# Kernel tuning notes

Hardware: AMD Instinct MI355X
Metric: run time of the kernel (lower is better)

The kernel has to match this reference:

```python
import jax, jax.numpy as jnp
import numpy as np

PROJ = 8192     # projDim
THRESH = 1e-8   # numerical-stability epsilon for signed sqrt
L2_EPS = 1e-12  # eps of torch F.normalize


def setup_inputs() -> dict:
    key = jax.random.key(0)
    k1, k2, k3, k4, k5 = jax.random.split(key, 5)
    B, C, H, W = 16, 512, 14, 14
    x = jax.random.normal(k1, (B, C, H, W), dtype=jnp.float32)
    h1 = jax.random.randint(k2, (C,), 0, PROJ, dtype=jnp.int32)
    h2 = jax.random.randint(k3, (C,), 0, PROJ, dtype=jnp.int32)
    s1 = (2 * jax.random.randint(k4, (C,), 0, 2) - 1).astype(jnp.float32)
    s2 = (2 * jax.random.randint(k5, (C,), 0, 2) - 1).astype(jnp.float32)
    return {"x": x, "s1": s1, "s2": s2, "h1": h1, "h2": h2}


def reference(x, s1, s2, h1, h2):
    # x: [B, C, H, W]; h*: [C] hash buckets in [0, PROJ); s*: [C] signs (+-1)
    B, C, H, W = x.shape
    x_flat = jnp.transpose(x, (0, 2, 3, 1)).reshape(-1, C)  # [N, C], N = B*H*W

    def count_sketch(s, h):
        # Equivalent to x_flat @ M with M[c, h[c]] = s[c]: scatter-add of
        # sign-weighted channels into PROJ bins.  -> [N, PROJ]
        return jax.ops.segment_sum((x_flat * s).T, h, num_segments=PROJ).T

    fft1 = jnp.fft.fft(count_sketch(s1, h1), axis=-1)
    fft2 = jnp.fft.fft(count_sketch(s2, h2), axis=-1)
    conv = jnp.fft.ifft(fft1 * fft2, axis=-1).real       # [N, PROJ]
    y = conv.reshape(B, H, W, PROJ).sum(axis=(1, 2))      # sum pool -> [B, PROJ]
    y = jnp.sign(y) * jnp.sqrt(jnp.abs(y) + THRESH)       # signed sqrt
    norm = jnp.linalg.norm(y, axis=1, keepdims=True)
    return y / jnp.maximum(norm, L2_EPS)                  # l2 normalize (dim=1)
```

## Files before the change

kernel.cpp:

```cpp
#include <hip/hip_runtime.h>
#include <math.h>

#define PROJ 8192
#define NB   16
#define NC   512
#define HW   196
#define NKC  7

typedef __attribute__((ext_vector_type(8))) short bf16x8;
typedef __attribute__((ext_vector_type(4))) float f32x4;

__device__ __forceinline__ unsigned bf16_rne(float f) {
    unsigned u = __builtin_bit_cast(unsigned, f);
    return (u + 0x7fffu + ((u >> 16) & 1u)) >> 16;
}

__device__ __forceinline__ void cvt_frag(const float4 f0, const float4 f1,
                                         const float s, bf16x8& hi, bf16x8& lo) {
    const float f[8] = {f0.x * s, f0.y * s, f0.z * s, f0.w * s,
                        f1.x * s, f1.y * s, f1.z * s, f1.w * s};
    bf16x8 h, l;
#pragma unroll
    for (int c = 0; c < 8; ++c) {
        const unsigned hu = bf16_rne(f[c]);
        h[c] = (short)hu;
        l[c] = (short)bf16_rne(f[c] - __builtin_bit_cast(float, hu << 16));
    }
    hi = h;
    lo = l;
}

__global__ __launch_bounds__(512, 2)
void cbp_gram(const float* __restrict__ x,
              const float* __restrict__ s1,
              const float* __restrict__ s2,
              const int*   __restrict__ h1,
              const int*   __restrict__ h2,
              float* __restrict__ ws) {
    __shared__ float sk[PROJ];
    __shared__ int   lh1[128], lh2[128];

    const int tid = threadIdx.x;
    const int blk = blockIdx.x;
    const int b    = 2 * (blk & 7) + (blk >> 7);
    const int tile = (blk >> 3) & 15;
    const int c1base = (tile >> 2) * 128;
    const int c2base = (tile & 3) * 128;

    const int lane = tid & 63;
    const int wave = tid >> 6;
    const int quad = lane >> 4;
    const int l15  = lane & 15;
    const int wr   = (wave >> 1) * 32;
    const int wc   = (wave & 1) * 64;

    for (int i = tid; i < PROJ; i += 512) sk[i] = 0.f;
    if (tid < 128) { lh1[tid] = h1[c1base + tid]; lh2[tid] = h2[c2base + tid]; }

    const float* xa = x + ((size_t)b * NC + c1base) * HW;
    const float* xb = x + ((size_t)b * NC + c2base) * HW;

    const float* pA[2]; float sa[2];
#pragma unroll
    for (int i = 0; i < 2; ++i) {
        const int r = wr + i * 16 + l15;
        pA[i] = xa + r * HW;
        sa[i] = s1[c1base + r];
    }
    const float* pB[4]; float sb[4];
#pragma unroll
    for (int j = 0; j < 4; ++j) {
        const int r = wc + j * 16 + l15;
        pB[j] = xb + r * HW;
        sb[j] = s2[c2base + r];
    }

    f32x4 acc[2][4];
#pragma unroll
    for (int i = 0; i < 2; ++i)
#pragma unroll
        for (int j = 0; j < 4; ++j) acc[i][j] = (f32x4){0.f, 0.f, 0.f, 0.f};

    const float4 z4 = {0.f, 0.f, 0.f, 0.f};
    float4 buf[2][12];

#define LOADC(par, kc) do {                                                   \
    const int kk_ = (kc) * 32 + quad * 8;                                     \
    const bool ok0_ = (kk_ + 3) < HW, ok1_ = (kk_ + 7) < HW;                  \
    _Pragma("unroll") for (int i_ = 0; i_ < 2; ++i_) {                        \
        buf[par][2*i_]   = ok0_ ? *(const float4*)(pA[i_] + kk_)     : z4;    \
        buf[par][2*i_+1] = ok1_ ? *(const float4*)(pA[i_] + kk_ + 4) : z4; }  \
    _Pragma("unroll") for (int j_ = 0; j_ < 4; ++j_) {                        \
        buf[par][4+2*j_]   = ok0_ ? *(const float4*)(pB[j_] + kk_)     : z4;  \
        buf[par][4+2*j_+1] = ok1_ ? *(const float4*)(pB[j_] + kk_ + 4) : z4; }\
} while (0)

    LOADC(0, 0);
#pragma unroll
    for (int kc = 0; kc < NKC; ++kc) {
        const int cur = kc & 1;
        if (kc + 1 < NKC) LOADC(cur ^ 1, kc + 1);

        bf16x8 ah[2], al[2], bh[4], bl[4];
#pragma unroll
        for (int i = 0; i < 2; ++i)
            cvt_frag(buf[cur][2*i], buf[cur][2*i+1], sa[i], ah[i], al[i]);
#pragma unroll
        for (int j = 0; j < 4; ++j)
            cvt_frag(buf[cur][4+2*j], buf[cur][4+2*j+1], sb[j], bh[j], bl[j]);

#pragma unroll
        for (int i = 0; i < 2; ++i)
#pragma unroll
            for (int j = 0; j < 4; ++j) {
                acc[i][j] = __builtin_amdgcn_mfma_f32_16x16x32_bf16(ah[i], bh[j], acc[i][j], 0, 0, 0);
                acc[i][j] = __builtin_amdgcn_mfma_f32_16x16x32_bf16(ah[i], bl[j], acc[i][j], 0, 0, 0);
                acc[i][j] = __builtin_amdgcn_mfma_f32_16x16x32_bf16(al[i], bh[j], acc[i][j], 0, 0, 0);
            }
    }
#undef LOADC

    __syncthreads();

#pragma unroll
    for (int i = 0; i < 2; ++i) {
        const int lr0 = wr + i * 16 + quad * 4;
#pragma unroll
        for (int j = 0; j < 4; ++j) {
            const int h2v = lh2[wc + j * 16 + l15];
#pragma unroll
            for (int rg = 0; rg < 4; ++rg) {
                const int bin = (lh1[lr0 + rg] + h2v) & (PROJ - 1);
                atomicAdd(&sk[bin], acc[i][j][rg]);
            }
        }
    }
    __syncthreads();

    float4* dst = (float4*)(ws + (size_t)blk * PROJ);
    const float4* src = (const float4*)sk;
    for (int i = tid; i < PROJ / 4; i += 512) dst[i] = src[i];
}

__device__ __forceinline__ float ssqrt(float s) {
    const float m = sqrtf(fabsf(s) + 1e-8f);
    return (s > 0.f) ? m : (s < 0.f ? -m : 0.f);
}

__global__ __launch_bounds__(512)
void cbp_finalize(const float* __restrict__ ws, float* __restrict__ y) {
    __shared__ float red[8];
    const int b   = blockIdx.x;
    const int tid = threadIdx.x;
    const int pbase = ((b & 1) << 7) | (b >> 1);

    float4 ov[4];
    float ssq = 0.f;
#pragma unroll
    for (int g = 0; g < 4; ++g) {
        const int f4 = tid + 512 * g;
        float4 s = {0.f, 0.f, 0.f, 0.f};
#pragma unroll
        for (int t = 0; t < 16; ++t) {
            const float4 v =
                ((const float4*)(ws + (size_t)(pbase | (t << 3)) * PROJ))[f4];
            s.x += v.x; s.y += v.y; s.z += v.z; s.w += v.w;
        }
        float4 o;
        o.x = ssqrt(s.x); o.y = ssqrt(s.y); o.z = ssqrt(s.z); o.w = ssqrt(s.w);
        ov[g] = o;
        ssq += o.x * o.x + o.y * o.y + o.z * o.z + o.w * o.w;
    }

    float v = ssq;
#pragma unroll
    for (int off = 32; off >= 1; off >>= 1) v += __shfl_xor(v, off, 64);
    if ((tid & 63) == 0) red[tid >> 6] = v;
    __syncthreads();
    float tot = 0.f;
#pragma unroll
    for (int w = 0; w < 8; ++w) tot += red[w];
    const float inv = 1.0f / fmaxf(sqrtf(tot), 1e-12f);

    float4* yp = (float4*)(y + (size_t)b * PROJ);
#pragma unroll
    for (int g = 0; g < 4; ++g) {
        float4 o = ov[g];
        o.x *= inv; o.y *= inv; o.z *= inv; o.w *= inv;
        yp[tid + 512 * g] = o;
    }
}

extern "C" void kernel_launch(void* const* d_in, const int* in_sizes, int n_in,
                              void* d_out, int out_size, void* d_ws, size_t ws_size,
                              hipStream_t stream) {
    const float* x  = (const float*)d_in[0];
    const float* s1 = (const float*)d_in[1];
    const float* s2 = (const float*)d_in[2];
    const int*   h1 = (const int*)d_in[3];
    const int*   h2 = (const int*)d_in[4];
    float* y  = (float*)d_out;
    float* ws = (float*)d_ws;

    hipLaunchKernelGGL(cbp_gram, dim3(256), dim3(512), 0, stream,
                       x, s1, s2, h1, h2, ws);
    hipLaunchKernelGGL(cbp_finalize, dim3(16), dim3(512), 0, stream, ws, y);
}
```

Measured before the change: 106.7 us.

## Precompute signed bf16 hi/lo splits in a separate conversion kernel

Adds a pre-pass kernel that multiplies x by the sign vectors once and writes bf16 hi/lo pairs for both sketches into a padded workspace layout. The gram kernel then loads ready-made bf16 fragments instead of converting fp32 data inside its inner loop. This removes the redundant per-tile conversion work, since each channel row was previously converted by four tiles. In exchange it adds an extra kernel launch and a round trip through global memory for the converted data, about 14.7 MB of bf16 arrays.

```diff
diff --git a/kernel.cpp b/kernel.cpp
--- a/kernel.cpp
+++ b/kernel.cpp
@@ -5,6 +5,7 @@
 #define NB   16
 #define NC   512
 #define HW   196
+#define KP   224
 #define NKC  7
 
 typedef __attribute__((ext_vector_type(8))) short bf16x8;
@@ -15,27 +16,52 @@
     return (u + 0x7fffu + ((u >> 16) & 1u)) >> 16;
 }
 
-__device__ __forceinline__ void cvt_frag(const float4 f0, const float4 f1,
-                                         const float s, bf16x8& hi, bf16x8& lo) {
-    const float f[8] = {f0.x * s, f0.y * s, f0.z * s, f0.w * s,
-                        f1.x * s, f1.y * s, f1.z * s, f1.w * s};
-    bf16x8 h, l;
-#pragma unroll
-    for (int c = 0; c < 8; ++c) {
-        const unsigned hu = bf16_rne(f[c]);
-        h[c] = (short)hu;
-        l[c] = (short)bf16_rne(f[c] - __builtin_bit_cast(float, hu << 16));
-    }
-    hi = h;
-    lo = l;
+__global__ __launch_bounds__(256)
+void cbp_convert(const float* __restrict__ x,
+                 const float* __restrict__ s1,
+                 const float* __restrict__ s2,
+                 short* __restrict__ X1h, short* __restrict__ X1l,
+                 short* __restrict__ X2h, short* __restrict__ X2l) {
+    const int v   = blockIdx.x * 256 + threadIdx.x;
+    const int b   = v / (NC * 28);
+    const int rem = v - b * (NC * 28);
+    const int c   = rem / 28;
+    const int g   = rem - c * 28;
+    const int kk  = g * 8;
+
+    const float* xs = x + ((size_t)b * NC + c) * HW;
+    float4 f0 = {0.f,0.f,0.f,0.f}, f1 = {0.f,0.f,0.f,0.f};
+    if (g < 24) {
+        f0 = *(const float4*)(xs + kk);
+        f1 = *(const float4*)(xs + kk + 4);
+    } else if (g == 24) {
+        f0 = *(const float4*)(xs + kk);
+    }
+    const float w1 = s1[c], w2 = s2[c];
+    const float f[8] = {f0.x, f0.y, f0.z, f0.w, f1.x, f1.y, f1.z, f1.w};
+    bf16x8 h1v, l1v, h2v, l2v;
+#pragma unroll
+    for (int e = 0; e < 8; ++e) {
+        const float a1 = f[e] * w1;
+        const unsigned u1 = bf16_rne(a1);
+        h1v[e] = (short)u1;
+        l1v[e] = (short)bf16_rne(a1 - __builtin_bit_cast(float, u1 << 16));
+        const float a2 = f[e] * w2;
+        const unsigned u2 = bf16_rne(a2);
+        h2v[e] = (short)u2;
+        l2v[e] = (short)bf16_rne(a2 - __builtin_bit_cast(float, u2 << 16));
+    }
+    const size_t off = ((size_t)b * NC + c) * KP + kk;
+    *(bf16x8*)(X1h + off) = h1v;
+    *(bf16x8*)(X1l + off) = l1v;
+    *(bf16x8*)(X2h + off) = h2v;
+    *(bf16x8*)(X2l + off) = l2v;
 }
 
 __global__ __launch_bounds__(512, 2)
-void cbp_gram(const float* __restrict__ x,
-              const float* __restrict__ s1,
-              const float* __restrict__ s2,
-              const int*   __restrict__ h1,
-              const int*   __restrict__ h2,
+void cbp_gram(const short* __restrict__ X1h, const short* __restrict__ X1l,
+              const short* __restrict__ X2h, const short* __restrict__ X2l,
+              const int*   __restrict__ h1,  const int*   __restrict__ h2,
               float* __restrict__ ws) {
     __shared__ float sk[PROJ];
     __shared__ int   lh1[128], lh2[128];
@@ -57,22 +83,17 @@
     for (int i = tid; i < PROJ; i += 512) sk[i] = 0.f;
     if (tid < 128) { lh1[tid] = h1[c1base + tid]; lh2[tid] = h2[c2base + tid]; }
 
-    const float* xa = x + ((size_t)b * NC + c1base) * HW;
-    const float* xb = x + ((size_t)b * NC + c2base) * HW;
-
-    const float* pA[2]; float sa[2];
+    const short* pAh[2]; const short* pAl[2];
 #pragma unroll
     for (int i = 0; i < 2; ++i) {
-        const int r = wr + i * 16 + l15;
-        pA[i] = xa + r * HW;
-        sa[i] = s1[c1base + r];
-    }
-    const float* pB[4]; float sb[4];
+        const size_t r = (size_t)(b * NC + c1base + wr + i * 16 + l15) * KP;
+        pAh[i] = X1h + r;  pAl[i] = X1l + r;
+    }
+    const short* pBh[4]; const short* pBl[4];
 #pragma unroll
     for (int j = 0; j < 4; ++j) {
-        const int r = wc + j * 16 + l15;
-        pB[j] = xb + r * HW;
-        sb[j] = s2[c2base + r];
+        const size_t r = (size_t)(b * NC + c2base + wc + j * 16 + l15) * KP;
+        pBh[j] = X2h + r;  pBl[j] = X2l + r;
     }
 
     f32x4 acc[2][4];
@@ -81,18 +102,16 @@
 #pragma unroll
         for (int j = 0; j < 4; ++j) acc[i][j] = (f32x4){0.f, 0.f, 0.f, 0.f};
 
-    const float4 z4 = {0.f, 0.f, 0.f, 0.f};
-    float4 buf[2][12];
+    bf16x8 buf[2][12];
 
 #define LOADC(par, kc) do {                                                   \
     const int kk_ = (kc) * 32 + quad * 8;                                     \
-    const bool ok0_ = (kk_ + 3) < HW, ok1_ = (kk_ + 7) < HW;                  \
     _Pragma("unroll") for (int i_ = 0; i_ < 2; ++i_) {                        \
-        buf[par][2*i_]   = ok0_ ? *(const float4*)(pA[i_] + kk_)     : z4;    \
-        buf[par][2*i_+1] = ok1_ ? *(const float4*)(pA[i_] + kk_ + 4) : z4; }  \
+        buf[par][2*i_]   = *(const bf16x8*)(pAh[i_] + kk_);                   \
+        buf[par][2*i_+1] = *(const bf16x8*)(pAl[i_] + kk_); }                 \
     _Pragma("unroll") for (int j_ = 0; j_ < 4; ++j_) {                        \
-        buf[par][4+2*j_]   = ok0_ ? *(const float4*)(pB[j_] + kk_)     : z4;  \
-        buf[par][4+2*j_+1] = ok1_ ? *(const float4*)(pB[j_] + kk_ + 4) : z4; }\
+        buf[par][4+2*j_]   = *(const bf16x8*)(pBh[j_] + kk_);                 \
+        buf[par][4+2*j_+1] = *(const bf16x8*)(pBl[j_] + kk_); }               \
 } while (0)
 
     LOADC(0, 0);
@@ -101,21 +120,15 @@
         const int cur = kc & 1;
         if (kc + 1 < NKC) LOADC(cur ^ 1, kc + 1);
 
-        bf16x8 ah[2], al[2], bh[4], bl[4];
 #pragma unroll
         for (int i = 0; i < 2; ++i)
-            cvt_frag(buf[cur][2*i], buf[cur][2*i+1], sa[i], ah[i], al[i]);
-#pragma unroll
-        for (int j = 0; j < 4; ++j)
-            cvt_frag(buf[cur][4+2*j], buf[cur][4+2*j+1], sb[j], bh[j], bl[j]);
-
-#pragma unroll
-        for (int i = 0; i < 2; ++i)
 #pragma unroll
             for (int j = 0; j < 4; ++j) {
-                acc[i][j] = __builtin_amdgcn_mfma_f32_16x16x32_bf16(ah[i], bh[j], acc[i][j], 0, 0, 0);
-                acc[i][j] = __builtin_amdgcn_mfma_f32_16x16x32_bf16(ah[i], bl[j], acc[i][j], 0, 0, 0);
-                acc[i][j] = __builtin_amdgcn_mfma_f32_16x16x32_bf16(al[i], bh[j], acc[i][j], 0, 0, 0);
+                const bf16x8 ah = buf[cur][2*i],     al = buf[cur][2*i+1];
+                const bf16x8 bh = buf[cur][4+2*j],   bl = buf[cur][4+2*j+1];
+                acc[i][j] = __builtin_amdgcn_mfma_f32_16x16x32_bf16(ah, bh, acc[i][j], 0, 0, 0);
+                acc[i][j] = __builtin_amdgcn_mfma_f32_16x16x32_bf16(ah, bl, acc[i][j], 0, 0, 0);
+                acc[i][j] = __builtin_amdgcn_mfma_f32_16x16x32_bf16(al, bh, acc[i][j], 0, 0, 0);
             }
     }
 #undef LOADC
@@ -202,7 +215,14 @@
     float* y  = (float*)d_out;
     float* ws = (float*)d_ws;
 
+    short* X1h = (short*)(ws + (size_t)256 * PROJ);
+    short* X1l = X1h + (size_t)NB * NC * KP;
+    short* X2h = X1l + (size_t)NB * NC * KP;
+    short* X2l = X2h + (size_t)NB * NC * KP;
+
+    hipLaunchKernelGGL(cbp_convert, dim3(896), dim3(256), 0, stream,
+                       x, s1, s2, X1h, X1l, X2h, X2l);
     hipLaunchKernelGGL(cbp_gram, dim3(256), dim3(512), 0, stream,
-                       x, s1, s2, h1, h2, ws);
+                       X1h, X1l, X2h, X2l, h1, h2, ws);
     hipLaunchKernelGGL(cbp_finalize, dim3(16), dim3(512), 0, stream, ws, y);
 }
```

Result: slower. 112.2 us (+5.1%).
